# Performance work log

Measured on AMD Instinct MI355X. Metric: run time of the kernel, lower is better.

Reference implementation:

```python
import jax, jax.numpy as jnp
import numpy as np

H = 1024
V_IN = 32000
V_OUT = 32000
MAX_LEN = 512
SOS = 0


def _gru_cell(x, h, W_ih, W_hh, b_ih, b_hh):
    # PyTorch GRU cell: gates ordered (r, z, n)
    gi = W_ih @ x + b_ih            # [3H]
    gh = W_hh @ h + b_hh            # [3H]
    i_r, i_z, i_n = jnp.split(gi, 3)
    h_r, h_z, h_n = jnp.split(gh, 3)
    r = jax.nn.sigmoid(i_r + h_r)
    z = jax.nn.sigmoid(i_z + h_z)
    n = jnp.tanh(i_n + r * h_n)
    return (1.0 - z) * n + z * h


def setup_inputs() -> dict:
    key = jax.random.key(0)
    ks = jax.random.split(key, 20)
    s = 0.02
    f = jnp.float32
    d = {}
    d["input_tensor"] = jax.random.randint(ks[0], (512,), 0, V_IN)
    d["target_tensor"] = jax.random.randint(ks[1], (512,), 0, V_OUT)
    d["enc_emb"] = jax.random.normal(ks[2], (V_IN, H), f) * s
    d["enc_W_ih"] = jax.random.normal(ks[3], (3 * H, H), f) * s
    d["enc_W_hh"] = jax.random.normal(ks[4], (3 * H, H), f) * s
    d["enc_b_ih"] = jnp.zeros((3 * H,), f)
    d["enc_b_hh"] = jnp.zeros((3 * H,), f)
    d["dec_emb"] = jax.random.normal(ks[5], (V_OUT, H), f) * s
    d["attn_W"] = jax.random.normal(ks[6], (MAX_LEN, 2 * H), f) * s
    d["attn_b"] = jnp.zeros((MAX_LEN,), f)
    d["comb_W"] = jax.random.normal(ks[7], (H, 2 * H), f) * s
    d["comb_b"] = jnp.zeros((H,), f)
    d["dec_W_ih"] = jax.random.normal(ks[8], (3 * H, H), f) * s
    d["dec_W_hh"] = jax.random.normal(ks[9], (3 * H, H), f) * s
    d["dec_b_ih"] = jnp.zeros((3 * H,), f)
    d["dec_b_hh"] = jnp.zeros((3 * H,), f)
    d["out_W"] = jax.random.normal(ks[10], (V_OUT, H), f) * s
    d["out_b"] = jnp.zeros((V_OUT,), f)
    return d


def reference(input_tensor, target_tensor, enc_emb, enc_W_ih, enc_W_hh,
              enc_b_ih, enc_b_hh, dec_emb, attn_W, attn_b, comb_W, comb_b,
              dec_W_ih, dec_W_hh, dec_b_ih, dec_b_hh, out_W, out_b):
    # --- encoder: per-token GRU ---
    def enc_step(h, tok):
        x = enc_emb[tok]
        h2 = _gru_cell(x, h, enc_W_ih, enc_W_hh, enc_b_ih, enc_b_hh)
        return h2, h2

    h0 = jnp.zeros((H,), enc_emb.dtype)
    h_final, enc_outs = jax.lax.scan(enc_step, h0, input_tensor)
    # zero-padded encoder memory of size max_length (as in original)
    enc_full = jnp.zeros((MAX_LEN, H), enc_outs.dtype).at[: enc_outs.shape[0]].set(enc_outs)

    # --- decoder (teacher forcing): inputs are [SOS, target[:-1]] ---
    dec_in = jnp.concatenate([jnp.array([SOS], dtype=target_tensor.dtype),
                              target_tensor[:-1]])

    def dec_step(h, inp):
        tok, tgt = inp
        e = dec_emb[tok]                                        # [H]
        aw = jax.nn.softmax(attn_W @ jnp.concatenate([e, h]) + attn_b)  # [MAX_LEN]
        applied = aw @ enc_full                                 # [H]
        x = jax.nn.relu(comb_W @ jnp.concatenate([e, applied]) + comb_b)
        h2 = _gru_cell(x, h, dec_W_ih, dec_W_hh, dec_b_ih, dec_b_hh)
        logp = jax.nn.log_softmax(out_W @ h2 + out_b)           # [V_OUT]
        return h2, -logp[tgt]

    _, nll = jax.lax.scan(dec_step, h_final, (dec_in, target_tensor))
    return jnp.sum(nll) / target_tensor.shape[0]
```

## Files before the change

### kernel.cpp

```cpp
#include <hip/hip_runtime.h>
#include <math.h>


#define H 1024
#define T 512
#define V 32000

typedef unsigned long long u64;

__device__ __forceinline__ void st_agent_f32(float* p, float v) {
    __hip_atomic_store(p, v, __ATOMIC_RELAXED, __HIP_MEMORY_SCOPE_AGENT);
}
__device__ __forceinline__ float2 ld_agent_f2(const float* p) {
    u64 u = __hip_atomic_load((const u64*)p, __ATOMIC_RELAXED,
                              __HIP_MEMORY_SCOPE_AGENT);
    float2 t;
    __builtin_memcpy(&t, &u, 8);
    return t;
}

__device__ __forceinline__ void grid_barrier(unsigned* cnts, unsigned target) {
    __syncthreads();
    if (threadIdx.x == 0) {
        __hip_atomic_fetch_add(cnts + ((blockIdx.x & 7) * 64), 1u,
                               __ATOMIC_RELAXED, __HIP_MEMORY_SCOPE_AGENT);
        unsigned sum;
        do {
            sum = 0;
            #pragma unroll
            for (int g = 0; g < 8; ++g)
                sum += __hip_atomic_load(cnts + g * 64, __ATOMIC_RELAXED,
                                         __HIP_MEMORY_SCOPE_AGENT);
        } while (sum < target);
        asm volatile("" ::: "memory");
    }
    __syncthreads();
}

__device__ __forceinline__ float sigmoidf_(float x) { return 1.f / (1.f + expf(-x)); }

__global__ __launch_bounds__(256) void gemm_tn(
    const float* __restrict__ X, int xs, int xo,
    const int* __restrict__ gidx, int gmode,
    const float* __restrict__ W, int wsd, int wo,
    const float* __restrict__ bias,
    float* __restrict__ C, int cs, int K)
{
    __shared__ float A_lds[32][64];
    __shared__ float B_lds[32][64];
    const int tid = threadIdx.x;
    const int tx = tid & 15, ty = tid >> 4;
    const int n0 = blockIdx.x * 64, t0 = blockIdx.y * 64;
    float acc[4][4] = {};

    for (int k0 = 0; k0 < K; k0 += 32) {
        #pragma unroll
        for (int q = 0; q < 2; ++q) {
            int f4 = tid + q * 256;
            int row = f4 >> 3, c4 = f4 & 7;
            int trow = t0 + row;
            const float* xr;
            if (gmode == 0)      xr = X + (size_t)trow * xs + xo;
            else if (gmode == 1) xr = X + (size_t)gidx[trow] * xs + xo;
            else { int tok = (trow == 0) ? 0 : gidx[trow - 1];
                   xr = X + (size_t)tok * xs + xo; }
            float4 a = *(const float4*)(xr + k0 + c4 * 4);
            A_lds[c4*4+0][row] = a.x; A_lds[c4*4+1][row] = a.y;
            A_lds[c4*4+2][row] = a.z; A_lds[c4*4+3][row] = a.w;
            const float* wr = W + (size_t)(n0 + row) * wsd + wo;
            float4 b = *(const float4*)(wr + k0 + c4 * 4);
            B_lds[c4*4+0][row] = b.x; B_lds[c4*4+1][row] = b.y;
            B_lds[c4*4+2][row] = b.z; B_lds[c4*4+3][row] = b.w;
        }
        __syncthreads();
        #pragma unroll
        for (int kk = 0; kk < 32; ++kk) {
            float4 a = *(const float4*)&A_lds[kk][ty * 4];
            float4 b = *(const float4*)&B_lds[kk][tx * 4];
            float av[4] = {a.x, a.y, a.z, a.w};
            float bv[4] = {b.x, b.y, b.z, b.w};
            #pragma unroll
            for (int i = 0; i < 4; ++i)
                #pragma unroll
                for (int j = 0; j < 4; ++j)
                    acc[i][j] = fmaf(av[i], bv[j], acc[i][j]);
        }
        __syncthreads();
    }
    float bj[4];
    #pragma unroll
    for (int j = 0; j < 4; ++j) bj[j] = bias ? bias[n0 + tx * 4 + j] : 0.f;
    #pragma unroll
    for (int i = 0; i < 4; ++i)
        #pragma unroll
        for (int j = 0; j < 4; ++j)
            C[(size_t)(t0 + ty * 4 + i) * cs + n0 + tx * 4 + j] = acc[i][j] + bj[j];
}

__global__ __launch_bounds__(512) void enc_seq(
    const float* __restrict__ Whh, const float* __restrict__ bhh,
    const float* __restrict__ gi,
    float* __restrict__ enc_outs,
    unsigned* __restrict__ bar)
{
    __shared__ float4 w4[12 * 256];
    __shared__ float h_lds[1024];
    __shared__ float gh_lds[12];
    __shared__ float bias_lds[12];
    const int tid = threadIdx.x, bid = blockIdx.x;
    const int j0 = bid * 4;
    for (int i = tid; i < 12 * 256; i += 512) {
        int r = i >> 8, c = i & 255;
        int grow = (r >> 2) * 1024 + j0 + (r & 3);
        w4[i] = *(const float4*)(Whh + (size_t)grow * 1024 + c * 4);
    }
    if (tid < 12) bias_lds[tid] = bhh[(tid >> 2) * 1024 + j0 + (tid & 3)];
    __syncthreads();

    const int wid = tid >> 6, lane = tid & 63;
    for (int t = 0; t < T; ++t) {
        if (t == 0) {
            if (tid < 256) ((float4*)h_lds)[tid] = make_float4(0.f, 0.f, 0.f, 0.f);
        } else {
            float2 hv = ld_agent_f2(enc_outs + (size_t)(t - 1) * 1024 + tid * 2);
            ((float2*)h_lds)[tid] = hv;
        }
        float gir = 0.f, giz = 0.f, gin = 0.f;
        if (tid < 4) {
            const float* gr = gi + (size_t)t * 3072 + j0 + tid;
            gir = gr[0]; giz = gr[1024]; gin = gr[2048];
        }
        __syncthreads();
        for (int rr = wid; rr < 12; rr += 8) {
            const float4* wrow = w4 + rr * 256;
            float acc = 0.f;
            #pragma unroll
            for (int i = 0; i < 4; ++i) {
                float4 wv = wrow[lane + 64 * i];
                float4 hv = ((const float4*)h_lds)[lane + 64 * i];
                acc += wv.x*hv.x + wv.y*hv.y + wv.z*hv.z + wv.w*hv.w;
            }
            #pragma unroll
            for (int o = 32; o; o >>= 1) acc += __shfl_xor(acc, o);
            if (lane == 0) gh_lds[rr] = acc + bias_lds[rr];
        }
        __syncthreads();
        if (tid < 4) {
            float r = sigmoidf_(gir + gh_lds[tid]);
            float z = sigmoidf_(giz + gh_lds[4 + tid]);
            float n = tanhf(gin + r * gh_lds[8 + tid]);
            float hp = h_lds[j0 + tid];
            st_agent_f32(enc_outs + (size_t)t * 1024 + j0 + tid,
                         (1.f - z) * n + z * hp);
        }
        if (t < T - 1) grid_barrier(bar, 256u * (unsigned)(t + 1));
    }
}

__global__ __launch_bounds__(512) void dec_seq(
    const float* __restrict__ Wih, const float* __restrict__ Whh,
    const float* __restrict__ bih, const float* __restrict__ bhh,
    const float* __restrict__ attnW,
    const float* __restrict__ attn_e,
    const float* __restrict__ comb_e,
    const float* __restrict__ M,
    const float* __restrict__ enc_outs,
    float* __restrict__ H2,
    float* __restrict__ s_buf, float* __restrict__ x_buf,
    unsigned* __restrict__ bar)
{
    __shared__ float4 wih4[12 * 256];
    __shared__ float4 whh4[12 * 256];
    __shared__ float4 aw4[2 * 256];
    __shared__ float4 m4[4 * 128];
    __shared__ float h_lds[1024];
    __shared__ float x_lds[1024];
    __shared__ float p_lds[512];
    __shared__ float gh_lds[12], gi_lds[12];
    __shared__ float bih_lds[12], bhh_lds[12];
    __shared__ float red[8];
    __shared__ float mx_sh, sum_sh;

    const int tid = threadIdx.x, bid = blockIdx.x;
    const int j0 = bid * 4, l0 = bid * 2;
    for (int i = tid; i < 12 * 256; i += 512) {
        int r = i >> 8, c = i & 255;
        int grow = (r >> 2) * 1024 + j0 + (r & 3);
        wih4[i] = *(const float4*)(Wih + (size_t)grow * 1024 + c * 4);
        whh4[i] = *(const float4*)(Whh + (size_t)grow * 1024 + c * 4);
    }
    for (int i = tid; i < 2 * 256; i += 512) {
        int r = i >> 8, c = i & 255;
        aw4[i] = *(const float4*)(attnW + (size_t)(l0 + r) * 2048 + 1024 + c * 4);
    }
    for (int i = tid; i < 4 * 128; i += 512) {
        int r = i >> 7, c = i & 127;
        m4[i] = *(const float4*)(M + (size_t)(j0 + r) * 512 + c * 4);
    }
    if (tid < 12) {
        int grow = (tid >> 2) * 1024 + j0 + (tid & 3);
        bih_lds[tid] = bih[grow]; bhh_lds[tid] = bhh[grow];
    }
    __syncthreads();

    const int wid = tid >> 6, lane = tid & 63;
    for (int t = 0; t < T; ++t) {
        const float* hsrc = (t == 0) ? (enc_outs + (size_t)(T - 1) * 1024)
                                     : (H2 + (size_t)(t - 1) * 1024);
        {
            float2 hv = ld_agent_f2(hsrc + tid * 2);
            ((float2*)h_lds)[tid] = hv;
        }
        float ae = 0.f;
        if ((wid == 4 || wid == 5) && lane == 0)
            ae = attn_e[(size_t)t * 512 + l0 + (wid - 4)];
        __syncthreads();
        for (int rr = wid; rr < 14; rr += 8) {
            const float4* wrow = (rr < 12) ? (whh4 + rr * 256) : (aw4 + (rr - 12) * 256);
            float acc = 0.f;
            #pragma unroll
            for (int i = 0; i < 4; ++i) {
                float4 wv = wrow[lane + 64 * i];
                float4 hv = ((const float4*)h_lds)[lane + 64 * i];
                acc += wv.x*hv.x + wv.y*hv.y + wv.z*hv.z + wv.w*hv.w;
            }
            #pragma unroll
            for (int o = 32; o; o >>= 1) acc += __shfl_xor(acc, o);
            if (lane == 0) {
                if (rr < 12) gh_lds[rr] = acc + bhh_lds[rr];
                else         st_agent_f32(s_buf + l0 + (rr - 12), acc + ae);
            }
        }
        grid_barrier(bar, 256u * (unsigned)(3 * t + 1));
        if (tid < 256) {
            float2 sv2 = ld_agent_f2(s_buf + tid * 2);
            ((float2*)p_lds)[tid] = sv2;
        }
        float ce = 0.f;
        if (wid < 4 && lane == 0) ce = comb_e[(size_t)t * 1024 + j0 + wid];
        __syncthreads();
        float v = p_lds[tid];
        float mv = v;
        #pragma unroll
        for (int o = 32; o; o >>= 1) mv = fmaxf(mv, __shfl_xor(mv, o));
        if (lane == 0) red[wid] = mv;
        __syncthreads();
        if (tid == 0) {
            float m2 = red[0];
            for (int w = 1; w < 8; ++w) m2 = fmaxf(m2, red[w]);
            mx_sh = m2;
        }
        __syncthreads();
        float e = expf(v - mx_sh);
        p_lds[tid] = e;
        float sv = e;
        #pragma unroll
        for (int o = 32; o; o >>= 1) sv += __shfl_xor(sv, o);
        if (lane == 0) red[wid] = sv;
        __syncthreads();
        if (tid == 0) {
            float s2 = 0.f;
            for (int w = 0; w < 8; ++w) s2 += red[w];
            sum_sh = s2;
        }
        __syncthreads();
        if (wid < 4) {
            const float4* mr = m4 + wid * 128;
            float acc = 0.f;
            #pragma unroll
            for (int i = 0; i < 2; ++i) {
                float4 mv4 = mr[lane + 64 * i];
                float4 pv4 = ((const float4*)p_lds)[lane + 64 * i];
                acc += mv4.x*pv4.x + mv4.y*pv4.y + mv4.z*pv4.z + mv4.w*pv4.w;
            }
            #pragma unroll
            for (int o = 32; o; o >>= 1) acc += __shfl_xor(acc, o);
            if (lane == 0) {
                float xv = ce + acc / sum_sh;
                st_agent_f32(x_buf + j0 + wid, fmaxf(xv, 0.f));
            }
        }
        grid_barrier(bar, 256u * (unsigned)(3 * t + 2));
        {
            float2 xv2 = ld_agent_f2(x_buf + tid * 2);
            ((float2*)x_lds)[tid] = xv2;
        }
        __syncthreads();
        for (int rr = wid; rr < 12; rr += 8) {
            const float4* wrow = wih4 + rr * 256;
            float acc = 0.f;
            #pragma unroll
            for (int i = 0; i < 4; ++i) {
                float4 wv = wrow[lane + 64 * i];
                float4 xv = ((const float4*)x_lds)[lane + 64 * i];
                acc += wv.x*xv.x + wv.y*xv.y + wv.z*xv.z + wv.w*xv.w;
            }
            #pragma unroll
            for (int o = 32; o; o >>= 1) acc += __shfl_xor(acc, o);
            if (lane == 0) gi_lds[rr] = acc + bih_lds[rr];
        }
        __syncthreads();
        if (tid < 4) {
            float r = sigmoidf_(gi_lds[tid] + gh_lds[tid]);
            float z = sigmoidf_(gi_lds[4 + tid] + gh_lds[4 + tid]);
            float n = tanhf(gi_lds[8 + tid] + r * gh_lds[8 + tid]);
            float hp = h_lds[j0 + tid];
            st_agent_f32(H2 + (size_t)t * 1024 + j0 + tid,
                         (1.f - z) * n + z * hp);
        }
        if (t < T - 1) grid_barrier(bar, 256u * (unsigned)(3 * t + 3));
    }
}

__global__ __launch_bounds__(256) void out_gemm_lse(
    const float* __restrict__ H2, const float* __restrict__ outW,
    const float* __restrict__ outB, const int* __restrict__ tgt,
    float* __restrict__ lsep, float* __restrict__ tgtlog)
{
    __shared__ float A_lds[32][128];
    __shared__ float B_lds[32][128];
    const int tid = threadIdx.x;
    const int tx = tid & 15, ty = tid >> 4;
    const int c0 = blockIdx.x * 128, r0 = blockIdx.y * 128;
    float acc[8][8] = {};

    for (int k0 = 0; k0 < 1024; k0 += 32) {
        #pragma unroll
        for (int q = 0; q < 4; ++q) {
            int f4 = tid + q * 256;
            int row = f4 >> 3, c4 = f4 & 7;
            float4 a = *(const float4*)(H2 + (size_t)(r0 + row) * 1024 + k0 + c4 * 4);
            A_lds[c4*4+0][row] = a.x; A_lds[c4*4+1][row] = a.y;
            A_lds[c4*4+2][row] = a.z; A_lds[c4*4+3][row] = a.w;
            float4 b = *(const float4*)(outW + (size_t)(c0 + row) * 1024 + k0 + c4 * 4);
            B_lds[c4*4+0][row] = b.x; B_lds[c4*4+1][row] = b.y;
            B_lds[c4*4+2][row] = b.z; B_lds[c4*4+3][row] = b.w;
        }
        __syncthreads();
        #pragma unroll
        for (int kk = 0; kk < 32; ++kk) {
            float4 a0 = *(const float4*)&A_lds[kk][ty * 8];
            float4 a1 = *(const float4*)&A_lds[kk][ty * 8 + 4];
            float4 b0 = *(const float4*)&B_lds[kk][tx * 8];
            float4 b1 = *(const float4*)&B_lds[kk][tx * 8 + 4];
            float av[8] = {a0.x,a0.y,a0.z,a0.w,a1.x,a1.y,a1.z,a1.w};
            float bv[8] = {b0.x,b0.y,b0.z,b0.w,b1.x,b1.y,b1.z,b1.w};
            #pragma unroll
            for (int i = 0; i < 8; ++i)
                #pragma unroll
                for (int j = 0; j < 8; ++j)
                    acc[i][j] = fmaf(av[i], bv[j], acc[i][j]);
        }
        __syncthreads();
    }
    float bj[8];
    #pragma unroll
    for (int j = 0; j < 8; ++j) bj[j] = outB[c0 + tx * 8 + j];

    const int bx = blockIdx.x;
    #pragma unroll
    for (int i = 0; i < 8; ++i) {
        int t = r0 + ty * 8 + i;
        float rowv[8];
        float vmax = -INFINITY;
        #pragma unroll
        for (int j = 0; j < 8; ++j) {
            rowv[j] = acc[i][j] + bj[j];
            vmax = fmaxf(vmax, rowv[j]);
        }
        float ssum = 0.f;
        #pragma unroll
        for (int j = 0; j < 8; ++j) ssum += expf(rowv[j] - vmax);
        #pragma unroll
        for (int o = 1; o < 16; o <<= 1) {
            float om = __shfl_xor(vmax, o);
            float os = __shfl_xor(ssum, o);
            float nm = fmaxf(vmax, om);
            ssum = ssum * expf(vmax - nm) + os * expf(om - nm);
            vmax = nm;
        }
        if (tx == 0)
            *(float2*)&lsep[((size_t)t * 250 + bx) * 2] = make_float2(vmax, ssum);
        int tv = tgt[t];
        if (tv >= c0 && tv < c0 + 128) {
            int rel = tv - c0;
            if ((rel >> 3) == tx) tgtlog[t] = rowv[rel & 7];
        }
    }
}

__global__ __launch_bounds__(512) void lse_combine(
    const float* __restrict__ lsep, const float* __restrict__ tgtlog,
    float* __restrict__ out)
{
    const int t = threadIdx.x;
    float m = -INFINITY, s = 0.f;
    for (int cb = 0; cb < 250; ++cb) {
        float2 p = *(const float2*)&lsep[((size_t)t * 250 + cb) * 2];
        float nm = fmaxf(m, p.x);
        s = s * expf(m - nm) + p.y * expf(p.x - nm);
        m = nm;
    }
    float nll = (m + logf(s)) - tgtlog[t];
    __shared__ float red[8];
    float v = nll;
    #pragma unroll
    for (int o = 32; o; o >>= 1) v += __shfl_xor(v, o);
    if ((t & 63) == 0) red[t >> 6] = v;
    __syncthreads();
    if (t == 0) {
        float sum = 0.f;
        for (int w = 0; w < 8; ++w) sum += red[w];
        out[0] = sum / 512.f;
    }
}

extern "C" void kernel_launch(void* const* d_in, const int* in_sizes, int n_in,
                              void* d_out, int out_size, void* d_ws, size_t ws_size,
                              hipStream_t stream) {
    const int*   input   = (const int*)d_in[0];
    const int*   target  = (const int*)d_in[1];
    const float* enc_emb = (const float*)d_in[2];
    const float* eWih    = (const float*)d_in[3];
    const float* eWhh    = (const float*)d_in[4];
    const float* ebih    = (const float*)d_in[5];
    const float* ebhh    = (const float*)d_in[6];
    const float* dec_emb = (const float*)d_in[7];
    const float* attnW   = (const float*)d_in[8];
    const float* attnB   = (const float*)d_in[9];
    const float* combW   = (const float*)d_in[10];
    const float* combB   = (const float*)d_in[11];
    const float* dWih    = (const float*)d_in[12];
    const float* dWhh    = (const float*)d_in[13];
    const float* dbih    = (const float*)d_in[14];
    const float* dbhh    = (const float*)d_in[15];
    const float* outW    = (const float*)d_in[16];
    const float* outB    = (const float*)d_in[17];
    float* out = (float*)d_out;

    float* wsf = (float*)d_ws;
    unsigned* barE = (unsigned*)d_ws;
    unsigned* barD = (unsigned*)((char*)d_ws + 4096);
    float* enc_gi   = wsf + 4096;
    float* enc_outs = wsf + 1576960;
    float* attn_e   = wsf + 2101248;
    float* comb_e   = wsf + 2363392;
    float* Mws      = wsf + 2887680;
    float* H2       = wsf + 3411968;
    float* s_buf    = wsf + 3936256;
    float* x_buf    = wsf + 3936768;
    float* lsep     = wsf + 3937792;
    float* tgtlog   = wsf + 4193792;

    hipMemsetAsync(d_ws, 0, 12288, stream);

    gemm_tn<<<dim3(48, 8), 256, 0, stream>>>(enc_emb, 1024, 0, input, 1,
        eWih, 1024, 0, ebih, enc_gi, 3072, 1024);
    gemm_tn<<<dim3(8, 8), 256, 0, stream>>>(dec_emb, 1024, 0, target, 2,
        attnW, 2048, 0, attnB, attn_e, 512, 1024);
    gemm_tn<<<dim3(16, 8), 256, 0, stream>>>(dec_emb, 1024, 0, target, 2,
        combW, 2048, 0, combB, comb_e, 1024, 1024);

    enc_seq<<<256, 512, 0, stream>>>(eWhh, ebhh, enc_gi, enc_outs, barE);

    gemm_tn<<<dim3(8, 16), 256, 0, stream>>>(combW, 2048, 1024, nullptr, 0,
        enc_outs, 1024, 0, nullptr, Mws, 512, 1024);

    dec_seq<<<256, 512, 0, stream>>>(dWih, dWhh, dbih, dbhh, attnW,
        attn_e, comb_e, Mws, enc_outs, H2, s_buf, x_buf, barD);

    out_gemm_lse<<<dim3(250, 4), 256, 0, stream>>>(H2, outW, outB, target,
        lsep, tgtlog);

    lse_combine<<<1, 512, 0, stream>>>(lsep, tgtlog, out);
}
```

Baseline: 7.673 ms.

## Replace counter grid barrier with per-block flag slots and overlap decoder gh work

Swaps the atomic-add counter barrier for per-block monotonic slot stores that one wavefront polls across all 256 blocks with a wave-wide all-check. This removes contention on the shared atomics. In the decoder, wave 0 alone runs the attention score, softmax and combine stages and their two inner grid syncs, while the other seven waves compute the W_hh gate products at the same time. This overlaps the hidden-state matvec with the serialized attention chain. The cost is that all softmax and combine work now sits on one wave, plus wider polling traffic.

```diff
diff --git a/kernel.cpp b/kernel.cpp
--- a/kernel.cpp
+++ b/kernel.cpp
@@ -18,23 +18,23 @@
     __builtin_memcpy(&t, &u, 8);
     return t;
 }
-
-__device__ __forceinline__ void grid_barrier(unsigned* cnts, unsigned target) {
-    __syncthreads();
-    if (threadIdx.x == 0) {
-        __hip_atomic_fetch_add(cnts + ((blockIdx.x & 7) * 64), 1u,
-                               __ATOMIC_RELAXED, __HIP_MEMORY_SCOPE_AGENT);
-        unsigned sum;
-        do {
-            sum = 0;
-            #pragma unroll
-            for (int g = 0; g < 8; ++g)
-                sum += __hip_atomic_load(cnts + g * 64, __ATOMIC_RELAXED,
-                                         __HIP_MEMORY_SCOPE_AGENT);
-        } while (sum < target);
-        asm volatile("" ::: "memory");
-    }
-    __syncthreads();
+__device__ __forceinline__ void st_slot(unsigned* p, unsigned v) {
+    __hip_atomic_store(p, v, __ATOMIC_RELAXED, __HIP_MEMORY_SCOPE_AGENT);
+}
+__device__ __forceinline__ unsigned ld_slot(const unsigned* p) {
+    return __hip_atomic_load(p, __ATOMIC_RELAXED, __HIP_MEMORY_SCOPE_AGENT);
+}
+
+__device__ __forceinline__ void poll_slots(const unsigned* slots, unsigned val,
+                                           int lane) {
+    for (;;) {
+        unsigned a = ld_slot(slots + (lane      ) * 16);
+        unsigned b = ld_slot(slots + (lane +  64) * 16);
+        unsigned c = ld_slot(slots + (lane + 128) * 16);
+        unsigned d = ld_slot(slots + (lane + 192) * 16);
+        int ok = (a >= val) & (b >= val) & (c >= val) & (d >= val);
+        if (__all(ok)) break;
+    }
 }
 
 __device__ __forceinline__ float sigmoidf_(float x) { return 1.f / (1.f + expf(-x)); }
@@ -101,7 +101,7 @@
     const float* __restrict__ Whh, const float* __restrict__ bhh,
     const float* __restrict__ gi,
     float* __restrict__ enc_outs,
-    unsigned* __restrict__ bar)
+    unsigned* __restrict__ slots)
 {
     __shared__ float4 w4[12 * 256];
     __shared__ float h_lds[1024];
@@ -122,8 +122,8 @@
         if (t == 0) {
             if (tid < 256) ((float4*)h_lds)[tid] = make_float4(0.f, 0.f, 0.f, 0.f);
         } else {
-            float2 hv = ld_agent_f2(enc_outs + (size_t)(t - 1) * 1024 + tid * 2);
-            ((float2*)h_lds)[tid] = hv;
+            ((float2*)h_lds)[tid] =
+                ld_agent_f2(enc_outs + (size_t)(t - 1) * 1024 + tid * 2);
         }
         float gir = 0.f, giz = 0.f, gin = 0.f;
         if (tid < 4) {
@@ -153,7 +153,14 @@
             st_agent_f32(enc_outs + (size_t)t * 1024 + j0 + tid,
                          (1.f - z) * n + z * hp);
         }
-        if (t < T - 1) grid_barrier(bar, 256u * (unsigned)(t + 1));
+        if (t < T - 1) {
+            if (wid == 0) {
+                asm volatile("s_waitcnt vmcnt(0)" ::: "memory");
+                if (lane == 0) st_slot(slots + bid * 16, (unsigned)(t + 1));
+                poll_slots(slots, (unsigned)(t + 1), lane);
+            }
+            __syncthreads();
+        }
     }
 }
 
@@ -167,7 +174,7 @@
     const float* __restrict__ enc_outs,
     float* __restrict__ H2,
     float* __restrict__ s_buf, float* __restrict__ x_buf,
-    unsigned* __restrict__ bar)
+    unsigned* __restrict__ slots)
 {
     __shared__ float4 wih4[12 * 256];
     __shared__ float4 whh4[12 * 256];
@@ -178,8 +185,6 @@
     __shared__ float p_lds[512];
     __shared__ float gh_lds[12], gi_lds[12];
     __shared__ float bih_lds[12], bhh_lds[12];
-    __shared__ float red[8];
-    __shared__ float mx_sh, sum_sh;
 
     const int tid = threadIdx.x, bid = blockIdx.x;
     const int j0 = bid * 4, l0 = bid * 2;
@@ -207,84 +212,91 @@
     for (int t = 0; t < T; ++t) {
         const float* hsrc = (t == 0) ? (enc_outs + (size_t)(T - 1) * 1024)
                                      : (H2 + (size_t)(t - 1) * 1024);
-        {
-            float2 hv = ld_agent_f2(hsrc + tid * 2);
-            ((float2*)h_lds)[tid] = hv;
-        }
-        float ae = 0.f;
-        if ((wid == 4 || wid == 5) && lane == 0)
-            ae = attn_e[(size_t)t * 512 + l0 + (wid - 4)];
-        __syncthreads();
-        for (int rr = wid; rr < 14; rr += 8) {
-            const float4* wrow = (rr < 12) ? (whh4 + rr * 256) : (aw4 + (rr - 12) * 256);
-            float acc = 0.f;
-            #pragma unroll
-            for (int i = 0; i < 4; ++i) {
-                float4 wv = wrow[lane + 64 * i];
-                float4 hv = ((const float4*)h_lds)[lane + 64 * i];
-                acc += wv.x*hv.x + wv.y*hv.y + wv.z*hv.z + wv.w*hv.w;
-            }
-            #pragma unroll
-            for (int o = 32; o; o >>= 1) acc += __shfl_xor(acc, o);
-            if (lane == 0) {
-                if (rr < 12) gh_lds[rr] = acc + bhh_lds[rr];
-                else         st_agent_f32(s_buf + l0 + (rr - 12), acc + ae);
-            }
-        }
-        grid_barrier(bar, 256u * (unsigned)(3 * t + 1));
-        if (tid < 256) {
-            float2 sv2 = ld_agent_f2(s_buf + tid * 2);
-            ((float2*)p_lds)[tid] = sv2;
-        }
-        float ce = 0.f;
-        if (wid < 4 && lane == 0) ce = comb_e[(size_t)t * 1024 + j0 + wid];
-        __syncthreads();
-        float v = p_lds[tid];
-        float mv = v;
-        #pragma unroll
-        for (int o = 32; o; o >>= 1) mv = fmaxf(mv, __shfl_xor(mv, o));
-        if (lane == 0) red[wid] = mv;
-        __syncthreads();
-        if (tid == 0) {
-            float m2 = red[0];
-            for (int w = 1; w < 8; ++w) m2 = fmaxf(m2, red[w]);
-            mx_sh = m2;
-        }
-        __syncthreads();
-        float e = expf(v - mx_sh);
-        p_lds[tid] = e;
-        float sv = e;
-        #pragma unroll
-        for (int o = 32; o; o >>= 1) sv += __shfl_xor(sv, o);
-        if (lane == 0) red[wid] = sv;
-        __syncthreads();
-        if (tid == 0) {
-            float s2 = 0.f;
-            for (int w = 0; w < 8; ++w) s2 += red[w];
-            sum_sh = s2;
-        }
-        __syncthreads();
-        if (wid < 4) {
-            const float4* mr = m4 + wid * 128;
-            float acc = 0.f;
-            #pragma unroll
-            for (int i = 0; i < 2; ++i) {
-                float4 mv4 = mr[lane + 64 * i];
-                float4 pv4 = ((const float4*)p_lds)[lane + 64 * i];
-                acc += mv4.x*pv4.x + mv4.y*pv4.y + mv4.z*pv4.z + mv4.w*pv4.w;
-            }
-            #pragma unroll
-            for (int o = 32; o; o >>= 1) acc += __shfl_xor(acc, o);
-            if (lane == 0) {
-                float xv = ce + acc / sum_sh;
-                st_agent_f32(x_buf + j0 + wid, fmaxf(xv, 0.f));
-            }
-        }
-        grid_barrier(bar, 256u * (unsigned)(3 * t + 2));
-        {
-            float2 xv2 = ld_agent_f2(x_buf + tid * 2);
-            ((float2*)x_lds)[tid] = xv2;
-        }
+        ((float2*)h_lds)[tid] = ld_agent_f2(hsrc + tid * 2);
+        float ae = 0.f, ce = 0.f;
+        if (wid == 0 && (lane & 31) == 0)
+            ae = attn_e[(size_t)t * 512 + l0 + (lane >> 5)];
+        if (wid == 0 && (lane & 15) == 0)
+            ce = comb_e[(size_t)t * 1024 + j0 + (lane >> 4)];
+        __syncthreads();
+
+        if (wid == 0) {
+            {
+                int r = lane >> 5, q2 = lane & 31;
+                const float4* arow = aw4 + r * 256;
+                float acc = 0.f;
+                #pragma unroll
+                for (int i = 0; i < 8; ++i) {
+                    float4 wv = arow[q2 + 32 * i];
+                    float4 hv = ((const float4*)h_lds)[q2 + 32 * i];
+                    acc += wv.x*hv.x + wv.y*hv.y + wv.z*hv.z + wv.w*hv.w;
+                }
+                #pragma unroll
+                for (int o = 16; o; o >>= 1) acc += __shfl_xor(acc, o);
+                if (q2 == 0) st_agent_f32(s_buf + l0 + r, acc + ae);
+            }
+            asm volatile("s_waitcnt vmcnt(0)" ::: "memory");
+            if (lane == 0) st_slot(slots + bid * 16, (unsigned)(3 * t + 1));
+            poll_slots(slots, (unsigned)(3 * t + 1), lane);
+
+            float sv[8];
+            {
+                float2 v0 = ld_agent_f2(s_buf + lane * 8);
+                float2 v1 = ld_agent_f2(s_buf + lane * 8 + 2);
+                float2 v2 = ld_agent_f2(s_buf + lane * 8 + 4);
+                float2 v3 = ld_agent_f2(s_buf + lane * 8 + 6);
+                sv[0]=v0.x; sv[1]=v0.y; sv[2]=v1.x; sv[3]=v1.y;
+                sv[4]=v2.x; sv[5]=v2.y; sv[6]=v3.x; sv[7]=v3.y;
+            }
+            float mx = sv[0];
+            #pragma unroll
+            for (int j = 1; j < 8; ++j) mx = fmaxf(mx, sv[j]);
+            #pragma unroll
+            for (int o = 32; o; o >>= 1) mx = fmaxf(mx, __shfl_xor(mx, o));
+            float pv[8], ssum = 0.f;
+            #pragma unroll
+            for (int j = 0; j < 8; ++j) { pv[j] = expf(sv[j] - mx); ssum += pv[j]; }
+            #pragma unroll
+            for (int o = 32; o; o >>= 1) ssum += __shfl_xor(ssum, o);
+            ((float4*)p_lds)[lane * 2]     = make_float4(pv[0], pv[1], pv[2], pv[3]);
+            ((float4*)p_lds)[lane * 2 + 1] = make_float4(pv[4], pv[5], pv[6], pv[7]);
+            asm volatile("s_waitcnt lgkmcnt(0)" ::: "memory");
+            {
+                int d = lane >> 4, q = lane & 15;
+                const float4* mr = m4 + d * 128;
+                float acc = 0.f;
+                #pragma unroll
+                for (int i = 0; i < 8; ++i) {
+                    float4 mv = mr[q + 16 * i];
+                    float4 pp = ((const float4*)p_lds)[q + 16 * i];
+                    acc += mv.x*pp.x + mv.y*pp.y + mv.z*pp.z + mv.w*pp.w;
+                }
+                #pragma unroll
+                for (int o = 8; o; o >>= 1) acc += __shfl_xor(acc, o);
+                if (q == 0)
+                    st_agent_f32(x_buf + j0 + d, fmaxf(ce + acc / ssum, 0.f));
+            }
+            asm volatile("s_waitcnt vmcnt(0)" ::: "memory");
+            if (lane == 0) st_slot(slots + bid * 16, (unsigned)(3 * t + 2));
+            poll_slots(slots, (unsigned)(3 * t + 2), lane);
+        } else {
+            for (int rr = wid - 1; rr < 12; rr += 7) {
+                const float4* wrow = whh4 + rr * 256;
+                float acc = 0.f;
+                #pragma unroll
+                for (int i = 0; i < 4; ++i) {
+                    float4 wv = wrow[lane + 64 * i];
+                    float4 hv = ((const float4*)h_lds)[lane + 64 * i];
+                    acc += wv.x*hv.x + wv.y*hv.y + wv.z*hv.z + wv.w*hv.w;
+                }
+                #pragma unroll
+                for (int o = 32; o; o >>= 1) acc += __shfl_xor(acc, o);
+                if (lane == 0) gh_lds[rr] = acc + bhh_lds[rr];
+            }
+        }
+        __syncthreads();
+
+        ((float2*)x_lds)[tid] = ld_agent_f2(x_buf + tid * 2);
         __syncthreads();
         for (int rr = wid; rr < 12; rr += 8) {
             const float4* wrow = wih4 + rr * 256;
@@ -308,7 +320,14 @@
             st_agent_f32(H2 + (size_t)t * 1024 + j0 + tid,
                          (1.f - z) * n + z * hp);
         }
-        if (t < T - 1) grid_barrier(bar, 256u * (unsigned)(3 * t + 3));
+        if (t < T - 1) {
+            if (wid == 0) {
+                asm volatile("s_waitcnt vmcnt(0)" ::: "memory");
+                if (lane == 0) st_slot(slots + bid * 16, (unsigned)(3 * t + 3));
+                poll_slots(slots, (unsigned)(3 * t + 3), lane);
+            }
+            __syncthreads();
+        }
     }
 }
 
@@ -439,20 +458,20 @@
     float* out = (float*)d_out;
 
     float* wsf = (float*)d_ws;
-    unsigned* barE = (unsigned*)d_ws;
-    unsigned* barD = (unsigned*)((char*)d_ws + 4096);
-    float* enc_gi   = wsf + 4096;
-    float* enc_outs = wsf + 1576960;
-    float* attn_e   = wsf + 2101248;
-    float* comb_e   = wsf + 2363392;
-    float* Mws      = wsf + 2887680;
-    float* H2       = wsf + 3411968;
-    float* s_buf    = wsf + 3936256;
-    float* x_buf    = wsf + 3936768;
-    float* lsep     = wsf + 3937792;
-    float* tgtlog   = wsf + 4193792;
-
-    hipMemsetAsync(d_ws, 0, 12288, stream);
+    unsigned* slotsE = (unsigned*)d_ws;
+    unsigned* slotsD = (unsigned*)((char*)d_ws + 16384);
+    float* enc_gi   = wsf + 8192;
+    float* enc_outs = wsf + 1581056;
+    float* attn_e   = wsf + 2105344;
+    float* comb_e   = wsf + 2367488;
+    float* Mws      = wsf + 2891776;
+    float* H2       = wsf + 3416064;
+    float* s_buf    = wsf + 3940352;
+    float* x_buf    = wsf + 3940864;
+    float* lsep     = wsf + 3941888;
+    float* tgtlog   = wsf + 4197888;
+
+    hipMemsetAsync(d_ws, 0, 32768, stream);
 
     gemm_tn<<<dim3(48, 8), 256, 0, stream>>>(enc_emb, 1024, 0, input, 1,
         eWih, 1024, 0, ebih, enc_gi, 3072, 1024);
@@ -461,13 +480,13 @@
     gemm_tn<<<dim3(16, 8), 256, 0, stream>>>(dec_emb, 1024, 0, target, 2,
         combW, 2048, 0, combB, comb_e, 1024, 1024);
 
-    enc_seq<<<256, 512, 0, stream>>>(eWhh, ebhh, enc_gi, enc_outs, barE);
+    enc_seq<<<256, 512, 0, stream>>>(eWhh, ebhh, enc_gi, enc_outs, slotsE);
 
     gemm_tn<<<dim3(8, 16), 256, 0, stream>>>(combW, 2048, 1024, nullptr, 0,
         enc_outs, 1024, 0, nullptr, Mws, 512, 1024);
 
     dec_seq<<<256, 512, 0, stream>>>(dWih, dWhh, dbih, dbhh, attnW,
-        attn_e, comb_e, Mws, enc_outs, H2, s_buf, x_buf, barD);
+        attn_e, comb_e, Mws, enc_outs, H2, s_buf, x_buf, slotsD);
 
     out_gemm_lse<<<dim3(250, 4), 256, 0, stream>>>(H2, outW, outB, target,
         lsep, tgtlog);
```

New measurement: 7.380 ms. -3.8%, faster.
